# Performance work log

Hardware: AMD Instinct MI355X
Metric: run time of the kernel (lower is better)

The kernel has to match this reference:

```python
import jax, jax.numpy as jnp
import numpy as np

DT_RANK = 64
D_STATE = 16


def setup_inputs() -> dict:
    key = jax.random.key(0)
    ks = jax.random.split(key, 6)
    B, L, Di = 2, 2048, 2048
    x = jax.random.normal(ks[0], (B, L, Di), dtype=jnp.float32)
    W_xproj = jax.random.normal(ks[1], (DT_RANK + 2 * D_STATE, Di), dtype=jnp.float32) * (Di ** -0.5)
    W_dt = jax.random.uniform(ks[2], (Di, DT_RANK), dtype=jnp.float32, minval=-(DT_RANK ** -0.5), maxval=DT_RANK ** -0.5)
    dt = jnp.exp(jax.random.uniform(ks[3], (Di,), dtype=jnp.float32) * (np.log(0.1) - np.log(0.001)) + np.log(0.001))
    b_dt = dt + jnp.log(-jnp.expm1(-dt))
    A_log = jnp.log(jnp.broadcast_to(jnp.arange(1, D_STATE + 1, dtype=jnp.float32), (Di, D_STATE)))
    D_param = jnp.ones((Di,), dtype=jnp.float32)
    return {"x": x, "W_xproj": W_xproj, "W_dt": W_dt, "b_dt": b_dt, "A_log": A_log, "D_param": D_param}


def _selective_scan(u, delta, A, Bm, Cm):
    # u, delta: (b, l, d); A: (d, n); Bm, Cm: (b, l, n)
    deltaA = jnp.exp(delta[..., None] * A[None, None])          # (b, l, d, n)
    deltaB_u = delta[..., None] * Bm[:, :, None, :] * u[..., None]  # (b, l, d, n)

    def step(h, inp):
        dA, dBu, c = inp                      # dA,dBu: (b,d,n); c: (b,n)
        h = dA * h + dBu
        y = jnp.einsum('bdn,bn->bd', h, c)
        return h, y

    b, l, d = u.shape
    h0 = jnp.zeros((b, d, A.shape[1]), dtype=u.dtype)
    xs = (jnp.moveaxis(deltaA, 1, 0), jnp.moveaxis(deltaB_u, 1, 0), jnp.moveaxis(Cm, 1, 0))
    _, ys = jax.lax.scan(step, h0, xs)        # ys: (l, b, d)
    return jnp.moveaxis(ys, 0, 1)


def reference(x, W_xproj, W_dt, b_dt, A_log, D_param):
    x_dbl = jnp.einsum('bld,ed->ble', x, W_xproj)  # (b, l, dt_rank + 2*n)
    dlt = x_dbl[..., :DT_RANK]
    Bm = x_dbl[..., DT_RANK:DT_RANK + D_STATE]
    Cm = x_dbl[..., DT_RANK + D_STATE:]
    delta = jax.nn.softplus(jnp.einsum('blr,dr->bld', dlt, W_dt) + b_dt)
    A = -jnp.exp(A_log.astype(jnp.float32))
    y = _selective_scan(x, delta, A, Bm, Cm)
    return y + x * D_param[None, None, :]
```

## Files before the change

kernel.cpp:

```cpp
#include <hip/hip_runtime.h>

#define BATCH 2
#define L_SEQ 2048
#define DI 2048
#define NROW (BATCH * L_SEQ)
#define E_DIM 96
#define RNK 64
#define NST 16
#define NCH 64
#define CL 32
#define SPLITK 16
#define KSL (DI / SPLITK)

#define WS_XDBL 0
#define WS_PART 393216
#define WS_HLOC 393216
#define WS_DSUM (393216 + 4194304)

__device__ __forceinline__ float softplusf(float z) {
    return fmaxf(z, 0.f) + __logf(1.f + __expf(-fabsf(z)));
}

__global__ __launch_bounds__(256) void gemm_xproj_part(const float* __restrict__ x,
                                                       const float* __restrict__ Wx,
                                                       float* __restrict__ part) {
    __shared__ float xs[32][68];
    __shared__ float wsh[32][100];
    const int tid = threadIdx.x;
    const int r0 = blockIdx.x * 64;
    const int kbase0 = blockIdx.y * KSL;
    const int rg = tid >> 4;
    const int cg = tid & 15;

    float acc[4][6];
#pragma unroll
    for (int i = 0; i < 4; i++)
#pragma unroll
        for (int j = 0; j < 6; j++) acc[i][j] = 0.f;

    for (int kt = 0; kt < KSL / 32; kt++) {
        const int kb = kbase0 + kt * 32;
#pragma unroll
        for (int rep = 0; rep < 2; rep++) {
            int i = rep * 256 + tid;
            int row = i >> 3;
            int kq = i & 7;
            float4 v = *(const float4*)&x[(long)(r0 + row) * DI + kb + kq * 4];
            xs[kq * 4 + 0][row] = v.x;
            xs[kq * 4 + 1][row] = v.y;
            xs[kq * 4 + 2][row] = v.z;
            xs[kq * 4 + 3][row] = v.w;
        }
#pragma unroll
        for (int rep = 0; rep < 3; rep++) {
            int i = rep * 256 + tid;
            int e = i >> 3;
            int kq = i & 7;
            float4 v = *(const float4*)&Wx[(long)e * DI + kb + kq * 4];
            wsh[kq * 4 + 0][e] = v.x;
            wsh[kq * 4 + 1][e] = v.y;
            wsh[kq * 4 + 2][e] = v.z;
            wsh[kq * 4 + 3][e] = v.w;
        }
        __syncthreads();
#pragma unroll 8
        for (int k = 0; k < 32; k++) {
            float xr[4], wr[6];
#pragma unroll
            for (int i = 0; i < 4; i++) xr[i] = xs[k][rg * 4 + i];
#pragma unroll
            for (int j = 0; j < 6; j++) wr[j] = wsh[k][cg * 6 + j];
#pragma unroll
            for (int i = 0; i < 4; i++)
#pragma unroll
                for (int j = 0; j < 6; j++) acc[i][j] = fmaf(xr[i], wr[j], acc[i][j]);
        }
        __syncthreads();
    }
    const long sbase = (long)blockIdx.y * NROW * E_DIM;
#pragma unroll
    for (int i = 0; i < 4; i++) {
        long rowb = sbase + (long)(r0 + rg * 4 + i) * E_DIM + cg * 6;
#pragma unroll
        for (int j = 0; j < 6; j++) part[rowb + j] = acc[i][j];
    }
}

__global__ __launch_bounds__(256) void xproj_reduce(const float* __restrict__ part,
                                                    float* __restrict__ xdbl) {
    const int i4 = blockIdx.x * 256 + threadIdx.x;
    const float4* p4 = (const float4*)part;
    float4 s = p4[i4];
#pragma unroll
    for (int sp = 1; sp < SPLITK; sp++) {
        float4 v = p4[(long)sp * (NROW * E_DIM / 4) + i4];
        s.x += v.x; s.y += v.y; s.z += v.z; s.w += v.w;
    }
    ((float4*)xdbl)[i4] = s;
}

__global__ __launch_bounds__(256) void gemm_dt(const float* __restrict__ xdbl,
                                               const float* __restrict__ Wdt,
                                               const float* __restrict__ b_dt,
                                               float* __restrict__ delta) {
    __shared__ float dl[32][68];
    __shared__ float wt[32][132];
    const int tid = threadIdx.x;
    const int row0 = blockIdx.x * 64;
    const int d0 = blockIdx.y * 128;
    const int rg = tid >> 5;
    const int cg = tid & 31;

    float acc[8][4];
#pragma unroll
    for (int i = 0; i < 8; i++)
#pragma unroll
        for (int j = 0; j < 4; j++) acc[i][j] = 0.f;

    for (int kt = 0; kt < 2; kt++) {
        const int kb = kt * 32;
#pragma unroll
        for (int rep = 0; rep < 2; rep++) {
            int i = rep * 256 + tid;
            int row = i >> 3;
            int kq = i & 7;
            float4 v = *(const float4*)&xdbl[(long)(row0 + row) * E_DIM + kb + kq * 4];
            dl[kq * 4 + 0][row] = v.x;
            dl[kq * 4 + 1][row] = v.y;
            dl[kq * 4 + 2][row] = v.z;
            dl[kq * 4 + 3][row] = v.w;
        }
#pragma unroll
        for (int rep = 0; rep < 4; rep++) {
            int i = rep * 256 + tid;
            int col = i >> 3;
            int kq = i & 7;
            float4 v = *(const float4*)&Wdt[(long)(d0 + col) * RNK + kb + kq * 4];
            wt[kq * 4 + 0][col] = v.x;
            wt[kq * 4 + 1][col] = v.y;
            wt[kq * 4 + 2][col] = v.z;
            wt[kq * 4 + 3][col] = v.w;
        }
        __syncthreads();
#pragma unroll 8
        for (int k = 0; k < 32; k++) {
            float xr[8], wr[4];
#pragma unroll
            for (int i = 0; i < 8; i++) xr[i] = dl[k][rg * 8 + i];
#pragma unroll
            for (int j = 0; j < 4; j++) wr[j] = wt[k][cg * 4 + j];
#pragma unroll
            for (int i = 0; i < 8; i++)
#pragma unroll
                for (int j = 0; j < 4; j++) acc[i][j] = fmaf(xr[i], wr[j], acc[i][j]);
        }
        __syncthreads();
    }

    float4 bb = *(const float4*)&b_dt[d0 + cg * 4];
#pragma unroll
    for (int i = 0; i < 8; i++) {
        int row = row0 + rg * 8 + i;
        float4 o;
        o.x = softplusf(acc[i][0] + bb.x);
        o.y = softplusf(acc[i][1] + bb.y);
        o.z = softplusf(acc[i][2] + bb.z);
        o.w = softplusf(acc[i][3] + bb.w);
        *(float4*)&delta[(long)row * DI + d0 + cg * 4] = o;
    }
}

__global__ __launch_bounds__(256) void scan_carry(const float* __restrict__ x,
                                                  const float* __restrict__ delta,
                                                  const float* __restrict__ xdbl,
                                                  const float* __restrict__ A_log,
                                                  float* __restrict__ hloc,
                                                  float* __restrict__ dsumb) {
    __shared__ float bs[CL * NST];
    const int tid = threadIdx.x;
    const int d = blockIdx.x * 256 + tid;
    const int c = blockIdx.y;
    const int b = blockIdx.z;
    const int row0 = b * L_SEQ + c * CL;

    for (int i = tid; i < CL * NST / 4; i += 256) {
        int row = i >> 2, q = i & 3;
        ((float4*)bs)[i] = *(const float4*)&xdbl[(long)(row0 + row) * E_DIM + 64 + q * 4];
    }
    __syncthreads();

    float A[16];
#pragma unroll
    for (int q = 0; q < 4; q++) {
        float4 v = *(const float4*)&A_log[(long)d * NST + q * 4];
        A[q * 4 + 0] = -__expf(v.x);
        A[q * 4 + 1] = -__expf(v.y);
        A[q * 4 + 2] = -__expf(v.z);
        A[q * 4 + 3] = -__expf(v.w);
    }
    float h[16];
#pragma unroll
    for (int n = 0; n < 16; n++) h[n] = 0.f;
    float dsum = 0.f;

    long idx = (long)row0 * DI + d;
    float dn = delta[idx], xn = x[idx];
    for (int ll = 0; ll < CL; ll++) {
        float dc = dn, xc = xn;
        if (ll + 1 < CL) { dn = delta[idx + DI]; xn = x[idx + DI]; }
        float du = dc * xc;
        float bl[16];
#pragma unroll
        for (int q = 0; q < 4; q++) {
            float4 v = *(const float4*)&bs[ll * NST + q * 4];
            bl[q * 4 + 0] = v.x; bl[q * 4 + 1] = v.y; bl[q * 4 + 2] = v.z; bl[q * 4 + 3] = v.w;
        }
#pragma unroll
        for (int n = 0; n < 16; n++)
            h[n] = fmaf(__expf(dc * A[n]), h[n], du * bl[n]);
        dsum += dc;
        idx += DI;
    }

    const long cb = ((long)(b * NCH + c) * DI + d);
#pragma unroll
    for (int q = 0; q < 4; q++)
        *(float4*)&hloc[cb * 16 + q * 4] =
            make_float4(h[q * 4], h[q * 4 + 1], h[q * 4 + 2], h[q * 4 + 3]);
    dsumb[cb] = dsum;
}

__global__ __launch_bounds__(256) void scan_prefix(const float* __restrict__ A_log,
                                                   float* __restrict__ hloc,
                                                   const float* __restrict__ dsumb) {
    const int g = blockIdx.x * 256 + threadIdx.x;
    const int n = g & 15;
    const int d = (g >> 4) & (DI - 1);
    const int b = g >> 15;
    const float An = -__expf(A_log[(long)d * NST + n]);
    float hc = 0.f;
    for (int c = 0; c < NCH; c++) {
        const long cb = ((long)(b * NCH + c) * DI + d);
        float hl = hloc[cb * 16 + n];
        float dsv = dsumb[cb];
        hloc[cb * 16 + n] = hc;
        hc = fmaf(__expf(An * dsv), hc, hl);
    }
}

__global__ __launch_bounds__(256) void scan_out(const float* __restrict__ x,
                                                const float* __restrict__ xdbl,
                                                const float* __restrict__ A_log,
                                                const float* __restrict__ Dp,
                                                const float* __restrict__ hloc,
                                                float* __restrict__ out) {
    __shared__ float bs[CL * NST];
    __shared__ float cs[CL * NST];
    const int tid = threadIdx.x;
    const int d = blockIdx.x * 256 + tid;
    const int c = blockIdx.y;
    const int b = blockIdx.z;
    const int row0 = b * L_SEQ + c * CL;

    for (int i = tid; i < CL * NST / 4; i += 256) {
        int row = i >> 2, q = i & 3;
        ((float4*)bs)[i] = *(const float4*)&xdbl[(long)(row0 + row) * E_DIM + 64 + q * 4];
        ((float4*)cs)[i] = *(const float4*)&xdbl[(long)(row0 + row) * E_DIM + 80 + q * 4];
    }
    __syncthreads();

    float A[16];
#pragma unroll
    for (int q = 0; q < 4; q++) {
        float4 v = *(const float4*)&A_log[(long)d * NST + q * 4];
        A[q * 4 + 0] = -__expf(v.x);
        A[q * 4 + 1] = -__expf(v.y);
        A[q * 4 + 2] = -__expf(v.z);
        A[q * 4 + 3] = -__expf(v.w);
    }
    float h[16];
    const long cb = ((long)(b * NCH + c) * DI + d);
#pragma unroll
    for (int q = 0; q < 4; q++) {
        float4 v = *(const float4*)&hloc[cb * 16 + q * 4];
        h[q * 4 + 0] = v.x; h[q * 4 + 1] = v.y; h[q * 4 + 2] = v.z; h[q * 4 + 3] = v.w;
    }
    const float Dd = Dp[d];

    long idx = (long)row0 * DI + d;
    float dn = out[idx], xn = x[idx];
    for (int ll = 0; ll < CL; ll++) {
        float dc = dn, xc = xn;
        if (ll + 1 < CL) { dn = out[idx + DI]; xn = x[idx + DI]; }
        float du = dc * xc;
        float y = 0.f;
#pragma unroll
        for (int q = 0; q < 4; q++) {
            float4 v = *(const float4*)&bs[ll * NST + q * 4];
            float4 w = *(const float4*)&cs[ll * NST + q * 4];
            float e0 = __expf(dc * A[q * 4 + 0]);
            float e1 = __expf(dc * A[q * 4 + 1]);
            float e2 = __expf(dc * A[q * 4 + 2]);
            float e3 = __expf(dc * A[q * 4 + 3]);
            h[q * 4 + 0] = fmaf(e0, h[q * 4 + 0], du * v.x);
            h[q * 4 + 1] = fmaf(e1, h[q * 4 + 1], du * v.y);
            h[q * 4 + 2] = fmaf(e2, h[q * 4 + 2], du * v.z);
            h[q * 4 + 3] = fmaf(e3, h[q * 4 + 3], du * v.w);
            y = fmaf(h[q * 4 + 0], w.x, y);
            y = fmaf(h[q * 4 + 1], w.y, y);
            y = fmaf(h[q * 4 + 2], w.z, y);
            y = fmaf(h[q * 4 + 3], w.w, y);
        }
        out[idx] = fmaf(xc, Dd, y);
        idx += DI;
    }
}

extern "C" void kernel_launch(void* const* d_in, const int* in_sizes, int n_in,
                              void* d_out, int out_size, void* d_ws, size_t ws_size,
                              hipStream_t stream) {
    const float* x    = (const float*)d_in[0];
    const float* Wx   = (const float*)d_in[1];
    const float* Wdt  = (const float*)d_in[2];
    const float* bdt  = (const float*)d_in[3];
    const float* Alog = (const float*)d_in[4];
    const float* Dp   = (const float*)d_in[5];
    float* out = (float*)d_out;
    float* ws = (float*)d_ws;
    float* xdbl  = ws + WS_XDBL;
    float* partb = ws + WS_PART;
    float* hloc  = ws + WS_HLOC;
    float* dsumb = ws + WS_DSUM;

    gemm_xproj_part<<<dim3(NROW / 64, SPLITK), 256, 0, stream>>>(x, Wx, partb);
    xproj_reduce<<<dim3(NROW * E_DIM / 4 / 256), 256, 0, stream>>>(partb, xdbl);
    gemm_dt<<<dim3(NROW / 64, DI / 128), 256, 0, stream>>>(xdbl, Wdt, bdt, out);
    scan_carry<<<dim3(DI / 256, NCH, BATCH), 256, 0, stream>>>(x, out, xdbl, Alog, hloc, dsumb);
    scan_prefix<<<dim3(BATCH * DI * NST / 256), 256, 0, stream>>>(Alog, hloc, dsumb);
    scan_out<<<dim3(DI / 256, NCH, BATCH), 256, 0, stream>>>(x, xdbl, Alog, Dp, hloc, out);
}
```

Measured before the change: 204.2 us.

## Fuse dt GEMM into chunk scan and stage scan inputs via LDS

Merges the delta projection GEMM with the per-chunk carry scan so that each block computes softplus(delta) for a 32x256 tile, keeps it in LDS and scans it immediately. This avoids re-reading delta from global memory in the carry kernel. The x and delta tiles for the carry and output scans are now loaded with global_load_lds into shared memory instead of per-step strided global loads. The prefix scan is restructured to batch all 64 chunk loads up front into registers and write to a separate hent buffer. The trade-offs are large LDS use, which lowers occupancy, and heavy register use in the prefix kernel.

```diff
diff --git a/kernel.cpp b/kernel.cpp
--- a/kernel.cpp
+++ b/kernel.cpp
@@ -16,9 +16,15 @@
 #define WS_PART 393216
 #define WS_HLOC 393216
 #define WS_DSUM (393216 + 4194304)
+#define WS_HENT (393216 + 6291456)
 
 __device__ __forceinline__ float softplusf(float z) {
     return fmaxf(z, 0.f) + __logf(1.f + __expf(-fabsf(z)));
+}
+
+__device__ __forceinline__ void glds16(const float* g, float* l) {
+    __builtin_amdgcn_global_load_lds((const __attribute__((address_space(1))) void*)g,
+                                     (__attribute__((address_space(3))) void*)l, 16, 0, 0);
 }
 
 __global__ __launch_bounds__(256) void gemm_xproj_part(const float* __restrict__ x,
@@ -99,18 +105,42 @@
     ((float4*)xdbl)[i4] = s;
 }
 
-__global__ __launch_bounds__(256) void gemm_dt(const float* __restrict__ xdbl,
-                                               const float* __restrict__ Wdt,
-                                               const float* __restrict__ b_dt,
-                                               float* __restrict__ delta) {
-    __shared__ float dl[32][68];
-    __shared__ float wt[32][132];
+#define PW 260
+#define PD 36
+__global__ __launch_bounds__(256, 2) void gemm_dt_scan(const float* __restrict__ x,
+                                                       const float* __restrict__ xdbl,
+                                                       const float* __restrict__ Wdt,
+                                                       const float* __restrict__ b_dt,
+                                                       const float* __restrict__ A_log,
+                                                       float* __restrict__ delta,
+                                                       float* __restrict__ hloc,
+                                                       float* __restrict__ dsumb) {
+    __shared__ float xsh[CL * 256];
+    __shared__ float region[32 * PW + 32 * PD];
+    __shared__ float bsm[CL * NST];
+    float* wt  = region;
+    float* dlb = region + 32 * PW;
+    float* dtt = region;
+
     const int tid = threadIdx.x;
-    const int row0 = blockIdx.x * 64;
-    const int d0 = blockIdx.y * 128;
-    const int rg = tid >> 5;
-    const int cg = tid & 31;
-
+    const int d0 = blockIdx.x * 256;
+    const int c = blockIdx.y;
+    const int b = blockIdx.z;
+    const int row0 = b * L_SEQ + c * CL;
+    const int wv = tid >> 6, ln = tid & 63;
+
+#pragma unroll
+    for (int r8 = 0; r8 < 8; r8++) {
+        int r = wv * 8 + r8;
+        glds16(&x[(long)(row0 + r) * DI + d0 + ln * 4], &xsh[r * 256]);
+    }
+    if (tid < 128) {
+        int r = tid >> 2, q = tid & 3;
+        ((float4*)bsm)[tid] = *(const float4*)&xdbl[(long)(row0 + r) * E_DIM + 64 + q * 4];
+    }
+
+    const int rg = tid >> 6;
+    const int cg = tid & 63;
     float acc[8][4];
 #pragma unroll
     for (int i = 0; i < 8; i++)
@@ -120,35 +150,31 @@
     for (int kt = 0; kt < 2; kt++) {
         const int kb = kt * 32;
 #pragma unroll
-        for (int rep = 0; rep < 2; rep++) {
+        for (int rep = 0; rep < 8; rep++) {
             int i = rep * 256 + tid;
-            int row = i >> 3;
-            int kq = i & 7;
-            float4 v = *(const float4*)&xdbl[(long)(row0 + row) * E_DIM + kb + kq * 4];
-            dl[kq * 4 + 0][row] = v.x;
-            dl[kq * 4 + 1][row] = v.y;
-            dl[kq * 4 + 2][row] = v.z;
-            dl[kq * 4 + 3][row] = v.w;
-        }
-#pragma unroll
-        for (int rep = 0; rep < 4; rep++) {
-            int i = rep * 256 + tid;
-            int col = i >> 3;
-            int kq = i & 7;
+            int col = i >> 3, kq = i & 7;
             float4 v = *(const float4*)&Wdt[(long)(d0 + col) * RNK + kb + kq * 4];
-            wt[kq * 4 + 0][col] = v.x;
-            wt[kq * 4 + 1][col] = v.y;
-            wt[kq * 4 + 2][col] = v.z;
-            wt[kq * 4 + 3][col] = v.w;
+            wt[(kq * 4 + 0) * PW + col] = v.x;
+            wt[(kq * 4 + 1) * PW + col] = v.y;
+            wt[(kq * 4 + 2) * PW + col] = v.z;
+            wt[(kq * 4 + 3) * PW + col] = v.w;
+        }
+        {
+            int r = tid >> 3, kq = tid & 7;
+            float4 v = *(const float4*)&xdbl[(long)(row0 + r) * E_DIM + kb + kq * 4];
+            dlb[(kq * 4 + 0) * PD + r] = v.x;
+            dlb[(kq * 4 + 1) * PD + r] = v.y;
+            dlb[(kq * 4 + 2) * PD + r] = v.z;
+            dlb[(kq * 4 + 3) * PD + r] = v.w;
         }
         __syncthreads();
 #pragma unroll 8
         for (int k = 0; k < 32; k++) {
-            float xr[8], wr[4];
-#pragma unroll
-            for (int i = 0; i < 8; i++) xr[i] = dl[k][rg * 8 + i];
-#pragma unroll
-            for (int j = 0; j < 4; j++) wr[j] = wt[k][cg * 4 + j];
+            float4 xa = *(const float4*)&dlb[k * PD + rg * 8];
+            float4 xb = *(const float4*)&dlb[k * PD + rg * 8 + 4];
+            float4 wv4 = *(const float4*)&wt[k * PW + cg * 4];
+            float xr[8] = {xa.x, xa.y, xa.z, xa.w, xb.x, xb.y, xb.z, xb.w};
+            float wr[4] = {wv4.x, wv4.y, wv4.z, wv4.w};
 #pragma unroll
             for (int i = 0; i < 8; i++)
 #pragma unroll
@@ -160,35 +186,17 @@
     float4 bb = *(const float4*)&b_dt[d0 + cg * 4];
 #pragma unroll
     for (int i = 0; i < 8; i++) {
-        int row = row0 + rg * 8 + i;
+        int r = rg * 8 + i;
         float4 o;
         o.x = softplusf(acc[i][0] + bb.x);
         o.y = softplusf(acc[i][1] + bb.y);
         o.z = softplusf(acc[i][2] + bb.z);
         o.w = softplusf(acc[i][3] + bb.w);
-        *(float4*)&delta[(long)row * DI + d0 + cg * 4] = o;
-    }
-}
-
-__global__ __launch_bounds__(256) void scan_carry(const float* __restrict__ x,
-                                                  const float* __restrict__ delta,
-                                                  const float* __restrict__ xdbl,
-                                                  const float* __restrict__ A_log,
-                                                  float* __restrict__ hloc,
-                                                  float* __restrict__ dsumb) {
-    __shared__ float bs[CL * NST];
-    const int tid = threadIdx.x;
-    const int d = blockIdx.x * 256 + tid;
-    const int c = blockIdx.y;
-    const int b = blockIdx.z;
-    const int row0 = b * L_SEQ + c * CL;
-
-    for (int i = tid; i < CL * NST / 4; i += 256) {
-        int row = i >> 2, q = i & 3;
-        ((float4*)bs)[i] = *(const float4*)&xdbl[(long)(row0 + row) * E_DIM + 64 + q * 4];
-    }
-    __syncthreads();
-
+        *(float4*)&delta[(long)(row0 + r) * DI + d0 + cg * 4] = o;
+        *(float4*)&dtt[r * 256 + cg * 4] = o;
+    }
+
+    const int d = d0 + tid;
     float A[16];
 #pragma unroll
     for (int q = 0; q < 4; q++) {
@@ -198,30 +206,26 @@
         A[q * 4 + 2] = -__expf(v.z);
         A[q * 4 + 3] = -__expf(v.w);
     }
+    __syncthreads();
+
     float h[16];
 #pragma unroll
     for (int n = 0; n < 16; n++) h[n] = 0.f;
     float dsum = 0.f;
-
-    long idx = (long)row0 * DI + d;
-    float dn = delta[idx], xn = x[idx];
     for (int ll = 0; ll < CL; ll++) {
-        float dc = dn, xc = xn;
-        if (ll + 1 < CL) { dn = delta[idx + DI]; xn = x[idx + DI]; }
+        float dc = dtt[ll * 256 + tid];
+        float xc = xsh[ll * 256 + tid];
         float du = dc * xc;
-        float bl[16];
 #pragma unroll
         for (int q = 0; q < 4; q++) {
-            float4 v = *(const float4*)&bs[ll * NST + q * 4];
-            bl[q * 4 + 0] = v.x; bl[q * 4 + 1] = v.y; bl[q * 4 + 2] = v.z; bl[q * 4 + 3] = v.w;
-        }
-#pragma unroll
-        for (int n = 0; n < 16; n++)
-            h[n] = fmaf(__expf(dc * A[n]), h[n], du * bl[n]);
+            float4 v = *(const float4*)&bsm[ll * NST + q * 4];
+            h[q * 4 + 0] = fmaf(__expf(dc * A[q * 4 + 0]), h[q * 4 + 0], du * v.x);
+            h[q * 4 + 1] = fmaf(__expf(dc * A[q * 4 + 1]), h[q * 4 + 1], du * v.y);
+            h[q * 4 + 2] = fmaf(__expf(dc * A[q * 4 + 2]), h[q * 4 + 2], du * v.z);
+            h[q * 4 + 3] = fmaf(__expf(dc * A[q * 4 + 3]), h[q * 4 + 3], du * v.w);
+        }
         dsum += dc;
-        idx += DI;
-    }
-
+    }
     const long cb = ((long)(b * NCH + c) * DI + d);
 #pragma unroll
     for (int q = 0; q < 4; q++)
@@ -230,45 +234,66 @@
     dsumb[cb] = dsum;
 }
 
-__global__ __launch_bounds__(256) void scan_prefix(const float* __restrict__ A_log,
-                                                   float* __restrict__ hloc,
-                                                   const float* __restrict__ dsumb) {
+__global__ __launch_bounds__(256, 1) void scan_prefix(const float* __restrict__ A_log,
+                                                      const float* __restrict__ hloc,
+                                                      const float* __restrict__ dsumb,
+                                                      float* __restrict__ hent) {
     const int g = blockIdx.x * 256 + threadIdx.x;
     const int n = g & 15;
     const int d = (g >> 4) & (DI - 1);
     const int b = g >> 15;
     const float An = -__expf(A_log[(long)d * NST + n]);
+    const long hstr = (long)DI * NST;
+    const long hbase = (long)b * NCH * hstr + (long)d * NST + n;
+    const long dbase = (long)b * NCH * DI + d;
+    float hl[NCH], dsv[NCH];
+#pragma unroll
+    for (int cc = 0; cc < NCH; cc++) {
+        hl[cc] = hloc[hbase + cc * hstr];
+        dsv[cc] = dsumb[dbase + cc * DI];
+    }
+    float e[NCH];
+#pragma unroll
+    for (int cc = 0; cc < NCH; cc++) e[cc] = __expf(An * dsv[cc]);
     float hc = 0.f;
-    for (int c = 0; c < NCH; c++) {
-        const long cb = ((long)(b * NCH + c) * DI + d);
-        float hl = hloc[cb * 16 + n];
-        float dsv = dsumb[cb];
-        hloc[cb * 16 + n] = hc;
-        hc = fmaf(__expf(An * dsv), hc, hl);
-    }
-}
-
-__global__ __launch_bounds__(256) void scan_out(const float* __restrict__ x,
-                                                const float* __restrict__ xdbl,
-                                                const float* __restrict__ A_log,
-                                                const float* __restrict__ Dp,
-                                                const float* __restrict__ hloc,
-                                                float* __restrict__ out) {
-    __shared__ float bs[CL * NST];
-    __shared__ float cs[CL * NST];
+#pragma unroll
+    for (int cc = 0; cc < NCH; cc++) {
+        hent[hbase + cc * hstr] = hc;
+        hc = fmaf(e[cc], hc, hl[cc]);
+    }
+}
+
+__global__ __launch_bounds__(256, 2) void scan_out(const float* __restrict__ x,
+                                                   const float* __restrict__ xdbl,
+                                                   const float* __restrict__ A_log,
+                                                   const float* __restrict__ Dp,
+                                                   const float* __restrict__ hent,
+                                                   float* __restrict__ out) {
+    __shared__ float xsh[CL * 256];
+    __shared__ float dsh[CL * 256];
+    __shared__ float bsm[CL * NST];
+    __shared__ float csm[CL * NST];
     const int tid = threadIdx.x;
-    const int d = blockIdx.x * 256 + tid;
+    const int d0 = blockIdx.x * 256;
     const int c = blockIdx.y;
     const int b = blockIdx.z;
     const int row0 = b * L_SEQ + c * CL;
-
-    for (int i = tid; i < CL * NST / 4; i += 256) {
-        int row = i >> 2, q = i & 3;
-        ((float4*)bs)[i] = *(const float4*)&xdbl[(long)(row0 + row) * E_DIM + 64 + q * 4];
-        ((float4*)cs)[i] = *(const float4*)&xdbl[(long)(row0 + row) * E_DIM + 80 + q * 4];
-    }
-    __syncthreads();
-
+    const int wv = tid >> 6, ln = tid & 63;
+
+#pragma unroll
+    for (int r8 = 0; r8 < 8; r8++) {
+        int r = wv * 8 + r8;
+        glds16(&x[(long)(row0 + r) * DI + d0 + ln * 4], &xsh[r * 256]);
+        glds16(&out[(long)(row0 + r) * DI + d0 + ln * 4], &dsh[r * 256]);
+    }
+    {
+        int i = tid & 127, r = i >> 2, q = i & 3;
+        float4 v = *(const float4*)&xdbl[(long)(row0 + r) * E_DIM + 64 + ((tid >> 7) << 4) + q * 4];
+        if (tid < 128) ((float4*)bsm)[i] = v;
+        else           ((float4*)csm)[i] = v;
+    }
+
+    const int d = d0 + tid;
     float A[16];
 #pragma unroll
     for (int q = 0; q < 4; q++) {
@@ -282,22 +307,22 @@
     const long cb = ((long)(b * NCH + c) * DI + d);
 #pragma unroll
     for (int q = 0; q < 4; q++) {
-        float4 v = *(const float4*)&hloc[cb * 16 + q * 4];
+        float4 v = *(const float4*)&hent[cb * 16 + q * 4];
         h[q * 4 + 0] = v.x; h[q * 4 + 1] = v.y; h[q * 4 + 2] = v.z; h[q * 4 + 3] = v.w;
     }
     const float Dd = Dp[d];
+    __syncthreads();
 
     long idx = (long)row0 * DI + d;
-    float dn = out[idx], xn = x[idx];
     for (int ll = 0; ll < CL; ll++) {
-        float dc = dn, xc = xn;
-        if (ll + 1 < CL) { dn = out[idx + DI]; xn = x[idx + DI]; }
+        float dc = dsh[ll * 256 + tid];
+        float xc = xsh[ll * 256 + tid];
         float du = dc * xc;
         float y = 0.f;
 #pragma unroll
         for (int q = 0; q < 4; q++) {
-            float4 v = *(const float4*)&bs[ll * NST + q * 4];
-            float4 w = *(const float4*)&cs[ll * NST + q * 4];
+            float4 v = *(const float4*)&bsm[ll * NST + q * 4];
+            float4 w = *(const float4*)&csm[ll * NST + q * 4];
             float e0 = __expf(dc * A[q * 4 + 0]);
             float e1 = __expf(dc * A[q * 4 + 1]);
             float e2 = __expf(dc * A[q * 4 + 2]);
@@ -331,11 +356,12 @@
     float* partb = ws + WS_PART;
     float* hloc  = ws + WS_HLOC;
     float* dsumb = ws + WS_DSUM;
+    float* hent  = ws + WS_HENT;
 
     gemm_xproj_part<<<dim3(NROW / 64, SPLITK), 256, 0, stream>>>(x, Wx, partb);
     xproj_reduce<<<dim3(NROW * E_DIM / 4 / 256), 256, 0, stream>>>(partb, xdbl);
-    gemm_dt<<<dim3(NROW / 64, DI / 128), 256, 0, stream>>>(xdbl, Wdt, bdt, out);
-    scan_carry<<<dim3(DI / 256, NCH, BATCH), 256, 0, stream>>>(x, out, xdbl, Alog, hloc, dsumb);
-    scan_prefix<<<dim3(BATCH * DI * NST / 256), 256, 0, stream>>>(Alog, hloc, dsumb);
-    scan_out<<<dim3(DI / 256, NCH, BATCH), 256, 0, stream>>>(x, xdbl, Alog, Dp, hloc, out);
-}
+    gemm_dt_scan<<<dim3(DI / 256, NCH, BATCH), 256, 0, stream>>>(x, xdbl, Wdt, bdt, Alog,
+                                                                 out, hloc, dsumb);
+    scan_prefix<<<dim3(BATCH * DI * NST / 256), 256, 0, stream>>>(Alog, hloc, dsumb, hent);
+    scan_out<<<dim3(DI / 256, NCH, BATCH), 256, 0, stream>>>(x, xdbl, Alog, Dp, hent, out);
+}
```

Measured after the change: 207.9 us. About the same (+1.8%).
